# Kernel optimization log

Hardware: AMD Instinct MI355X
Metric: run time of the kernel (lower is better)

Reference implementation:

```python
import jax, jax.numpy as jnp
import numpy as np

B, IMG, TXT, DIM, H, D = 1, 1024, 256, 1536, 24, 64
SCALE = 1.0  # control cross-attn scale


def _lin(x, w, b):
    return x @ w + b


def _heads(x):  # [B,S,DIM] -> [B,H,S,D]
    return jnp.swapaxes(x.reshape(x.shape[0], x.shape[1], H, D), 1, 2)


def _merge(x):  # [B,H,S,D] -> [B,S,DIM]
    return jnp.swapaxes(x, 1, 2).reshape(x.shape[0], x.shape[2], H * D)


def _sdpa(q, k, v):
    s = jnp.einsum('bhqd,bhkd->bhqk', q, k) * (1.0 / np.sqrt(D))
    return jnp.einsum('bhqk,bhkd->bhqd', jax.nn.softmax(s, axis=-1), v)


def _rope(x, pe):  # x: [B,H,S,D], pe: [1,1,S,D//2,2,2]
    xr = x.reshape(*x.shape[:-1], -1, 1, 2)  # [B,H,S,D/2,1,2]
    out = pe[..., 0] * xr[..., 0] + pe[..., 1] * xr[..., 1]  # [B,H,S,D/2,2]
    return out.reshape(x.shape)


def _forward(hidden_states, encoder_hidden_states, hidden_states_control,
             encoder_hidden_states_control, img_to_q_control, pe,
             a_q_w, a_q_b, a_k_w, a_k_b, a_v_w, a_v_b,
             a_addq_w, a_addq_b, a_addk_w, a_addk_b, a_addv_w, a_addv_b,
             a_out_w, a_out_b, a_addout_w, a_addout_b,
             c_q_w, c_q_b, c_k_w, c_k_b, c_v_w, c_v_b,
             c_addq_w, c_addq_b, c_addk_w, c_addk_b, c_addv_w, c_addv_b,
             c_out_w, c_out_b, c_addout_w, c_addout_b):
    img_len = hidden_states.shape[1]
    # ---- main joint attention stream (no RoPE, per original) ----
    q = jnp.concatenate([_heads(_lin(hidden_states, a_q_w, a_q_b)),
                         _heads(_lin(encoder_hidden_states, a_addq_w, a_addq_b))], axis=2)
    k = jnp.concatenate([_heads(_lin(hidden_states, a_k_w, a_k_b)),
                         _heads(_lin(encoder_hidden_states, a_addk_w, a_addk_b))], axis=2)
    v = jnp.concatenate([_heads(_lin(hidden_states, a_v_w, a_v_b)),
                         _heads(_lin(encoder_hidden_states, a_addv_w, a_addv_b))], axis=2)
    hs = _merge(_sdpa(q, k, v))
    hs, ehs = hs[:, :img_len], hs[:, img_len:]
    # ---- control joint attention stream (with RoPE) ----
    qc = jnp.concatenate([_heads(_lin(hidden_states_control, c_q_w, c_q_b)),
                          _heads(_lin(encoder_hidden_states_control, c_addq_w, c_addq_b))], axis=2)
    kc = jnp.concatenate([_heads(_lin(hidden_states_control, c_k_w, c_k_b)),
                          _heads(_lin(encoder_hidden_states_control, c_addk_w, c_addk_b))], axis=2)
    vc = jnp.concatenate([_heads(_lin(hidden_states_control, c_v_w, c_v_b)),
                          _heads(_lin(encoder_hidden_states_control, c_addv_w, c_addv_b))], axis=2)
    key_cross, value_cross = kc, vc  # saved BEFORE RoPE, per original
    hsc = _merge(_sdpa(_rope(qc, pe), _rope(kc, pe), vc))
    hsc, ehsc = hsc[:, :img_len], hsc[:, img_len:]
    # ---- cross attention: img query attends to control K/V ----
    q_cross = _rope(_heads(img_to_q_control), pe[:, :, :img_len])
    k_cross = _rope(key_cross, pe[:, :, :key_cross.shape[2]])
    cross = _merge(_sdpa(q_cross, k_cross, value_cross))
    hs = hs + SCALE * cross
    # ---- output projections (to_out[1] is dropout p=0 -> identity) ----
    hs = _lin(hs, a_out_w, a_out_b)
    ehs = _lin(ehs, a_addout_w, a_addout_b)
    hsc = _lin(hsc, c_out_w, c_out_b)
    ehsc = _lin(ehsc, c_addout_w, c_addout_b)
    return hs, ehs, hsc, ehsc


def setup_inputs() -> dict:
    key = jax.random.key(0)
    ki = iter(jax.random.split(key, 80))
    d = {}
    d['hidden_states'] = jax.random.normal(next(ki), (B, IMG, DIM), jnp.float32)
    d['encoder_hidden_states'] = jax.random.normal(next(ki), (B, TXT, DIM), jnp.float32)
    d['hidden_states_control'] = jax.random.normal(next(ki), (B, IMG, DIM), jnp.float32)
    d['encoder_hidden_states_control'] = jax.random.normal(next(ki), (B, TXT, DIM), jnp.float32)
    d['img_to_q_control'] = jax.random.normal(next(ki), (B, IMG, DIM), jnp.float32)
    # realistic rotary pe: [1,1,S,D/2,2,2] rotation matrices
    S = IMG + TXT
    pos = np.arange(S, dtype=np.float32)
    freqs = 1.0 / (10000.0 ** (np.arange(0, D, 2, dtype=np.float32) / D))  # [D/2]
    ang = pos[:, None] * freqs[None, :]  # [S, D/2]
    cos, sin = np.cos(ang), np.sin(ang)
    pe = np.stack([np.stack([cos, -sin], -1), np.stack([sin, cos], -1)], -2)  # [S,D/2,2,2]
    d['pe'] = jnp.asarray(pe)[None, None]
    for p in ('a', 'c'):
        for name in ('q', 'k', 'v', 'addq', 'addk', 'addv', 'out', 'addout'):
            d[f'{p}_{name}_w'] = jax.random.normal(next(ki), (DIM, DIM), jnp.float32) * 0.02
            d[f'{p}_{name}_b'] = jax.random.normal(next(ki), (DIM,), jnp.float32) * 0.01
    return d


def reference(hidden_states, encoder_hidden_states, hidden_states_control,
              encoder_hidden_states_control, img_to_q_control, pe,
              a_q_w, a_q_b, a_k_w, a_k_b, a_v_w, a_v_b,
              a_addq_w, a_addq_b, a_addk_w, a_addk_b, a_addv_w, a_addv_b,
              a_out_w, a_out_b, a_addout_w, a_addout_b,
              c_q_w, c_q_b, c_k_w, c_k_b, c_v_w, c_v_b,
              c_addq_w, c_addq_b, c_addk_w, c_addk_b, c_addv_w, c_addv_b,
              c_out_w, c_out_b, c_addout_w, c_addout_b):
    return _forward(hidden_states, encoder_hidden_states, hidden_states_control,
                    encoder_hidden_states_control, img_to_q_control, pe,
                    a_q_w, a_q_b, a_k_w, a_k_b, a_v_w, a_v_b,
                    a_addq_w, a_addq_b, a_addk_w, a_addk_b, a_addv_w, a_addv_b,
                    a_out_w, a_out_b, a_addout_w, a_addout_b,
                    c_q_w, c_q_b, c_k_w, c_k_b, c_v_w, c_v_b,
                    c_addq_w, c_addq_b, c_addk_w, c_addk_b, c_addv_w, c_addv_b,
                    c_out_w, c_out_b, c_addout_w, c_addout_b)
```

## Files before the change

### kernel.cpp

```cpp
#include <hip/hip_runtime.h>

#define DIM 1536
#define IMG 1024
#define TXT 256
#define SEQ 1280
#define NH 24
#define HD 64
#define SD ((size_t)SEQ * DIM)
#define IDSZ ((size_t)IMG * DIM)
#define WSZ ((size_t)DIM * DIM)

typedef __attribute__((ext_vector_type(8))) short short8;
typedef __attribute__((ext_vector_type(4))) float f32x4;

__device__ __forceinline__ float bf2f(ushort u) {
    union { unsigned int i; float f; } v; v.i = ((unsigned int)u) << 16; return v.f;
}
__device__ __forceinline__ ushort f2bf(float f) {
    union { unsigned int i; float f; } v; v.f = f;
    unsigned int u = v.i;
    u += 0x7fffu + ((u >> 16) & 1u);
    return (ushort)(u >> 16);
}
__device__ __forceinline__ ushort f2bf_rz(float f) {
    union { unsigned int i; float f; } v; v.f = f;
    return (ushort)(v.i >> 16);
}

__global__ __launch_bounds__(256) void detect_dtype(const void* __restrict__ p,
                                                    int* __restrict__ flag)
{
    __shared__ int cnt;
    if (threadIdx.x == 0) cnt = 0;
    __syncthreads();
    const ushort* u = (const ushort*)p;
    int local = 0;
    for (int i = threadIdx.x; i < 2048; i += 256) {
        ushort v = u[2 * i];
        int e = (v >> 7) & 0xFF;
        if (e >= 0xC0) local++;
    }
    atomicAdd(&cnt, local);
    __syncthreads();
    if (threadIdx.x == 0) flag[0] = (cnt > 16) ? 1 : 0;
}

struct CvtP {
    const void* src[20];
    ushort* dst[20];
    int n8[20];
};

__global__ __launch_bounds__(256) void convert_bf16(CvtP p, const int* __restrict__ dflag)
{
    const int a = blockIdx.y;
    const int i = blockIdx.x * 256 + threadIdx.x;
    if (i >= p.n8[a]) return;
    const size_t off = (size_t)i * 8;
    uint4 o;
    if (dflag[0]) {
        const float* s = (const float*)p.src[a] + off;
        const float4 f0 = *(const float4*)s;
        const float4 f1 = *(const float4*)(s + 4);
        ushort t[8];
        t[0] = f2bf(f0.x); t[1] = f2bf(f0.y); t[2] = f2bf(f0.z); t[3] = f2bf(f0.w);
        t[4] = f2bf(f1.x); t[5] = f2bf(f1.y); t[6] = f2bf(f1.z); t[7] = f2bf(f1.w);
        o = *(uint4*)t;
    } else {
        o = *(const uint4*)((const ushort*)p.src[a] + off);
    }
    *(uint4*)(p.dst[a] + off) = o;
}

#define LSTR 40

struct QKV3P {
    const ushort* Xb;
    const ushort* Wb;
    const void* B[12];
    float* Y[6];
    ushort* Yh[6];
    ushort* Yl[6];
};

__global__ __launch_bounds__(256) void gemm_qkv_v4(QKV3P p, const int* __restrict__ dflag)
{
    __shared__ __align__(16) ushort As[2][128 * LSTR];
    __shared__ __align__(16) ushort Bs[2][64 * 64];
    const int dt = dflag[0];
    const int bx = blockIdx.x;
    const int wsel = bx / 12;
    const int n0 = (bx - wsel * 12) * 128;
    const int ys = blockIdx.y;
    const int str = (ys >= 10) ? 1 : 0;
    const int m0g = (ys - str * 10) * 128;
    const bool istxt = (m0g >= IMG);
    const int widx = str * 6 + wsel + (istxt ? 3 : 0);
    const ushort* X  = p.Xb + (size_t)str * SD;
    const ushort* Wp = p.Wb + (size_t)widx * WSZ;
    const void* Bp = p.B[widx];
    const int yidx = str * 3 + wsel;
    float*  Y  = p.Y[yidx];
    ushort* yh = p.Yh[yidx];
    ushort* yl = p.Yl[yidx];

    const int t = threadIdx.x;
    const int wave = t >> 6, lane = t & 63;
    const int quad = lane >> 4, l16 = lane & 15;
    const int wm = (wave >> 1) * 64, wn = (wave & 1) * 64;

    const int arow = t >> 1, apair = t & 1;
    const int bn8 = (t & 15) << 3, bkk = (t >> 4) << 1;
    const int aps = apair ^ ((arow >> 3) & 1);
    const int adst = arow * LSTR + aps * 16;
    const int bkg = bkk >> 3, bo = bkk & 7;

    f32x4 acc[4][4];
#pragma unroll
    for (int i = 0; i < 4; ++i)
#pragma unroll
        for (int j = 0; j < 4; ++j) acc[i][j] = (f32x4)(0.0f);

    uint4 rau[2];
    uint4 rbu[2];

    auto loadA = [&](int k0) {
        const ushort* xp = X + (size_t)(m0g + arow) * DIM + k0 + apair * 16;
        rau[0] = *(const uint4*)xp;
        rau[1] = *(const uint4*)(xp + 8);
    };
    auto loadB = [&](int k0) {
        const ushort* wp0 = Wp + (size_t)(k0 + bkk) * DIM + n0 + bn8;
        rbu[0] = *(const uint4*)wp0;
        rbu[1] = *(const uint4*)(wp0 + DIM);
    };
    auto storeA = [&](int buf) {
        *(uint4*)&As[buf][adst]     = rau[0];
        *(uint4*)&As[buf][adst + 8] = rau[1];
    };
    auto storeB = [&](int buf) {
        ushort t0[8], t1[8];
        *(uint4*)t0 = rbu[0];
        *(uint4*)t1 = rbu[1];
#pragma unroll
        for (int j = 0; j < 8; ++j) {
            const int rr = bn8 + j;
            const int R = rr & 63, half = rr >> 6;
            const int gx = (((half << 2) + bkg) ^ (R & 7) ^ (R >> 3)) & 7;
            *(unsigned int*)&Bs[buf][R * 64 + gx * 8 + bo] =
                (unsigned int)t0[j] | ((unsigned int)t1[j] << 16);
        }
    };

    loadA(0); loadB(0);
    storeA(0); storeB(0);
    __syncthreads();

    for (int k = 0; k < DIM / 32; ++k) {
        const int cur = k & 1;
        const bool hn = (k + 1) < DIM / 32;
        if (hn) { loadA((k + 1) * 32); loadB((k + 1) * 32); }

        short8 b[4];
#pragma unroll
        for (int j = 0; j < 4; ++j) {
            const int rrn = wn + j * 16 + l16;
            const int R = rrn & 63, half = rrn >> 6;
            const int gx = (((half << 2) + quad) ^ (R & 7) ^ (R >> 3)) & 7;
            b[j] = *(const short8*)&Bs[cur][R * 64 + gx * 8];
        }
#pragma unroll
        for (int i = 0; i < 4; ++i) {
            const int rr = wm + i * 16 + l16;
            const int ps = (quad >> 1) ^ ((rr >> 3) & 1);
            const int col = ps * 16 + (quad & 1) * 8;
            short8 a = *(const short8*)&As[cur][rr * LSTR + col];
#pragma unroll
            for (int j = 0; j < 4; ++j)
                acc[i][j] = __builtin_amdgcn_mfma_f32_16x16x32_bf16(a, b[j], acc[i][j], 0, 0, 0);
        }
        if (hn) { storeA(cur ^ 1); storeB(cur ^ 1); }
        __syncthreads();
    }

#pragma unroll
    for (int j = 0; j < 4; ++j) {
        const int col = n0 + wn + j * 16 + l16;
        const float bv = dt ? ((const float*)Bp)[col] : bf2f(((const ushort*)Bp)[col]);
#pragma unroll
        for (int i = 0; i < 4; ++i)
#pragma unroll
            for (int r = 0; r < 4; ++r) {
                const int row = m0g + wm + i * 16 + quad * 4 + r;
                const size_t o = (size_t)row * DIM + col;
                const float val = acc[i][j][r] + bv;
                if (Y) Y[o] = val;
                if (yh) {
                    const ushort hv = f2bf(val);
                    yh[o] = hv;
                    yl[o] = f2bf(val - bf2f(hv));
                }
            }
    }
}

struct OutP {
    const ushort* Xh; const ushort* Xl;
    const ushort* Wb;
    const void* B[4];
    void* out;
};

__global__ __launch_bounds__(256) void gemm_out_v4(OutP p, const int* __restrict__ dflag)
{
    __shared__ __align__(16) ushort Ah[2][64 * LSTR];
    __shared__ __align__(16) ushort Al[2][64 * LSTR];
    __shared__ __align__(16) ushort Bs[2][64 * 64];
    const int dt = dflag[0];
    const int n0 = blockIdx.x * 128;
    const int mt = blockIdx.y;
    const int seg = (mt < 16) ? 0 : (mt < 20) ? 1 : (mt < 36) ? 2 : 3;
    const ushort* Wp = p.Wb + (size_t)seg * WSZ;
    const void* Bp = p.B[seg];
    const int m0 = mt * 64;

    const int t = threadIdx.x;
    const int wave = t >> 6, lane = t & 63;
    const int quad = lane >> 4, l16 = lane & 15;
    const int wm = (wave >> 1) * 32, wn = (wave & 1) * 64;

    const int arow = t >> 2, ag = t & 3;
    const int apg = ag >> 1, asub = ag & 1;
    const int aps = apg ^ ((arow >> 3) & 1);
    const int adst = arow * LSTR + aps * 16 + asub * 8;
    const int bn8 = (t & 15) << 3, bkk = (t >> 4) << 1;
    const int bkg = bkk >> 3, bo = bkk & 7;

    f32x4 acc[2][4];
#pragma unroll
    for (int i = 0; i < 2; ++i)
#pragma unroll
        for (int j = 0; j < 4; ++j) acc[i][j] = (f32x4)(0.0f);

    uint4 rah, ral;
    uint4 rbu[2];

    auto loadA = [&](int k0) {
        const size_t off = (size_t)(m0 + arow) * DIM + k0 + ag * 8;
        rah = *(const uint4*)(p.Xh + off);
        ral = *(const uint4*)(p.Xl + off);
    };
    auto loadB = [&](int k0) {
        const ushort* wp0 = Wp + (size_t)(k0 + bkk) * DIM + n0 + bn8;
        rbu[0] = *(const uint4*)wp0;
        rbu[1] = *(const uint4*)(wp0 + DIM);
    };
    auto storeA = [&](int buf) {
        *(uint4*)&Ah[buf][adst] = rah;
        *(uint4*)&Al[buf][adst] = ral;
    };
    auto storeB = [&](int buf) {
        ushort t0[8], t1[8];
        *(uint4*)t0 = rbu[0];
        *(uint4*)t1 = rbu[1];
#pragma unroll
        for (int j = 0; j < 8; ++j) {
            const int rr = bn8 + j;
            const int R = rr & 63, half = rr >> 6;
            const int gx = (((half << 2) + bkg) ^ (R & 7) ^ (R >> 3)) & 7;
            *(unsigned int*)&Bs[buf][R * 64 + gx * 8 + bo] =
                (unsigned int)t0[j] | ((unsigned int)t1[j] << 16);
        }
    };

    loadA(0); loadB(0);
    storeA(0); storeB(0);
    __syncthreads();

    for (int k = 0; k < DIM / 32; ++k) {
        const int cur = k & 1;
        const bool hn = (k + 1) < DIM / 32;
        if (hn) { loadA((k + 1) * 32); loadB((k + 1) * 32); }

        short8 b[4];
#pragma unroll
        for (int j = 0; j < 4; ++j) {
            const int rrn = wn + j * 16 + l16;
            const int R = rrn & 63, half = rrn >> 6;
            const int gx = (((half << 2) + quad) ^ (R & 7) ^ (R >> 3)) & 7;
            b[j] = *(const short8*)&Bs[cur][R * 64 + gx * 8];
        }
#pragma unroll
        for (int i = 0; i < 2; ++i) {
            const int rr = wm + i * 16 + l16;
            const int ps = (quad >> 1) ^ ((rr >> 3) & 1);
            const int col = ps * 16 + (quad & 1) * 8;
            short8 ah = *(const short8*)&Ah[cur][rr * LSTR + col];
            short8 al = *(const short8*)&Al[cur][rr * LSTR + col];
#pragma unroll
            for (int j = 0; j < 4; ++j) {
                acc[i][j] = __builtin_amdgcn_mfma_f32_16x16x32_bf16(ah, b[j], acc[i][j], 0, 0, 0);
                acc[i][j] = __builtin_amdgcn_mfma_f32_16x16x32_bf16(al, b[j], acc[i][j], 0, 0, 0);
            }
        }
        if (hn) { storeA(cur ^ 1); storeB(cur ^ 1); }
        __syncthreads();
    }

#pragma unroll
    for (int j = 0; j < 4; ++j) {
        const int col = n0 + wn + j * 16 + l16;
        const float bv = dt ? ((const float*)Bp)[col] : bf2f(((const ushort*)Bp)[col]);
#pragma unroll
        for (int i = 0; i < 2; ++i)
#pragma unroll
            for (int r = 0; r < 4; ++r) {
                const int grow = m0 + wm + i * 16 + quad * 4 + r;
                const size_t o = (size_t)grow * DIM + col;
                const float val = acc[i][j][r] + bv;
                if (dt) ((float*)p.out)[o] = val;
                else    ((ushort*)p.out)[o] = f2bf(val);
            }
    }
}

__device__ __forceinline__ void pe_load(const void* pe, int dt, size_t off,
                                        float& c00, float& c01, float& c10, float& c11)
{
    if (dt) {
        float4 pv = *(const float4*)((const float*)pe + off);
        c00 = pv.x; c01 = pv.y; c10 = pv.z; c11 = pv.w;
    } else {
        const ushort* pp = (const ushort*)pe + off;
        c00 = bf2f(pp[0]); c01 = bf2f(pp[1]); c10 = bf2f(pp[2]); c11 = bf2f(pp[3]);
    }
}

struct PrepP {
    const float* v1; const float* vC;
    ushort *vthA, *vtlA, *vthC, *vtlC;
    float* q1;
    const float* k1; ushort *khC, *kloC;
    const void* i2q; float* qx;
    const void* pe;
};

#define VT_BLKS 960
#define RN0 (SEQ * 768)
#define RN1 (SEQ * 768)
#define RN2 (IMG * 768)

__global__ __launch_bounds__(256) void prep_fused(PrepP p, const int* __restrict__ dflag)
{
    __shared__ unsigned int tile[64 * 65];
    const int dt = dflag[0];
    const int bx = blockIdx.x;
    const int t = threadIdx.x;

    if (bx < VT_BLKS) {
        const int z = bx / 480, rem = bx - z * 480;
        const int s0 = (rem % 20) * 64, h = rem / 20;
        const float* V = z ? p.vC : p.v1;
        ushort* Vth = z ? p.vthC : p.vthA;
        ushort* Vtl = z ? p.vtlC : p.vtlA;
#pragma unroll
        for (int it = 0; it < 16; ++it) {
            const int sl = (t >> 6) + (it << 2);
            const int d = t & 63;
            const float v = V[(size_t)(s0 + sl) * DIM + h * HD + d];
            const ushort hv = f2bf(v);
            const ushort lv = f2bf(v - bf2f(hv));
            tile[d * 65 + sl] = (unsigned int)hv | ((unsigned int)lv << 16);
        }
        __syncthreads();
        const int d = t >> 2, cc = (t & 3) << 4;
        ushort th[16], tl[16];
#pragma unroll
        for (int j = 0; j < 16; ++j) {
            const unsigned int w = tile[d * 65 + cc + j];
            th[j] = (ushort)w;
            tl[j] = (ushort)(w >> 16);
        }
        const size_t off = (size_t)(h * HD + d) * SEQ + s0 + cc;
        *(uint4*)(Vth + off)     = *(uint4*)&th[0];
        *(uint4*)(Vth + off + 8) = *(uint4*)&th[8];
        *(uint4*)(Vtl + off)     = *(uint4*)&tl[0];
        *(uint4*)(Vtl + off + 8) = *(uint4*)&tl[8];
        return;
    }

    int idx = (bx - VT_BLKS) * 256 + t;
    if (idx < RN0) {
        int s = idx / 768, pp = idx - s * 768;
        int col = pp << 1, i = pp & 31;
        float* bp = p.q1 + (size_t)s * DIM + col;
        float x0 = bp[0], x1 = bp[1];
        float c00, c01, c10, c11;
        pe_load(p.pe, dt, (size_t)s * 128 + i * 4, c00, c01, c10, c11);
        bp[0] = c00 * x0 + c01 * x1;
        bp[1] = c10 * x0 + c11 * x1;
        return;
    }
    idx -= RN0;
    if (idx < RN1) {
        int s = idx / 768, pp = idx - s * 768;
        int col = pp << 1, i = pp & 31;
        float2 xv = *(const float2*)(p.k1 + (size_t)s * DIM + col);
        float c00, c01, c10, c11;
        pe_load(p.pe, dt, (size_t)s * 128 + i * 4, c00, c01, c10, c11);
        float y0 = c00 * xv.x + c01 * xv.y;
        float y1 = c10 * xv.x + c11 * xv.y;
        ushort h0 = f2bf(y0), h1 = f2bf(y1);
        ushort l0 = f2bf(y0 - bf2f(h0)), l1 = f2bf(y1 - bf2f(h1));
        *(unsigned int*)(p.khC  + (size_t)s * DIM + col) = (unsigned int)h0 | ((unsigned int)h1 << 16);
        *(unsigned int*)(p.kloC + (size_t)s * DIM + col) = (unsigned int)l0 | ((unsigned int)l1 << 16);
        return;
    }
    idx -= RN1;
    if (idx < RN2) {
        int s = idx / 768, pp = idx - s * 768;
        int col = pp << 1, i = pp & 31;
        float x0, x1;
        if (dt) {
            float2 xv = *(const float2*)((const float*)p.i2q + (size_t)s * DIM + col);
            x0 = xv.x; x1 = xv.y;
        } else {
            const ushort* sp = (const ushort*)p.i2q + (size_t)s * DIM + col;
            x0 = bf2f(sp[0]); x1 = bf2f(sp[1]);
        }
        float c00, c01, c10, c11;
        pe_load(p.pe, dt, (size_t)s * 128 + i * 4, c00, c01, c10, c11);
        float* dp = p.qx + (size_t)s * DIM + col;
        dp[0] = c00 * x0 + c01 * x1;
        dp[1] = c10 * x0 + c11 * x1;
    }
}

__device__ __forceinline__ int swz(int row, int col) {
    return row * 64 + ((((col >> 3) ^ row) & 7) << 3) + (col & 7);
}
__device__ __forceinline__ short8 ldfrag(const ushort* plane, int row, int col) {
    return *(const short8*)&plane[swz(row, col)];
}

struct AttnAllP {
    const float* Qf[3];
    const ushort* Kh[3]; const ushort* Kl[3];
    const ushort* Vth[3]; const ushort* Vtl[3];
    float* Op0[3]; float* Op1[3];
    float2* Ml[3];
    int mlq[3];
};

__global__ __launch_bounds__(256) void attn_all(AttnAllP p)
{
    __shared__ ushort Qh_[4096], Ql_[4096];
    __shared__ ushort Kh_[4096], Kl_[4096];
    __shared__ ushort Vh_[4096], Vl_[4096];

    const int bx = blockIdx.x;
    const int seg = (bx < 20) ? 0 : (bx < 40) ? 1 : 2;
    const int q0 = (bx - ((seg == 0) ? 0 : (seg == 1) ? 20 : 40)) * 64;
    const int h = blockIdx.y;
    const int z = blockIdx.z;
    const int t = threadIdx.x;
    const int wave = t >> 6, lane = t & 63;
    const int quad = lane >> 4, l16 = lane & 15;
    const int wq0 = wave * 16;

    const float* Qf = p.Qf[seg];
    const ushort* Kh = p.Kh[seg]; const ushort* Kl = p.Kl[seg];
    const ushort* Vth = p.Vth[seg]; const ushort* Vtl = p.Vtl[seg];

    const int srow = t >> 2, c0 = (t & 3) << 4;
    const int g0 = c0 >> 3;
    const int p0 = ((g0 ^ (srow & 7)) & 7) << 3;
    const int p1 = (((g0 + 1) ^ (srow & 7)) & 7) << 3;

    {
        const float* src = Qf + (size_t)(q0 + srow) * DIM + h * HD + c0;
        float x[16];
        *(float4*)&x[0]  = *(const float4*)(src);
        *(float4*)&x[4]  = *(const float4*)(src + 4);
        *(float4*)&x[8]  = *(const float4*)(src + 8);
        *(float4*)&x[12] = *(const float4*)(src + 12);
        ushort hi[16], lo[16];
#pragma unroll
        for (int i = 0; i < 16; ++i) {
            const float xs = x[i] * 0.125f;
            hi[i] = f2bf(xs);
            lo[i] = f2bf(xs - bf2f(hi[i]));
        }
        *(uint4*)&Qh_[srow * 64 + p0] = *(uint4*)&hi[0];
        *(uint4*)&Qh_[srow * 64 + p1] = *(uint4*)&hi[8];
        *(uint4*)&Ql_[srow * 64 + p0] = *(uint4*)&lo[0];
        *(uint4*)&Ql_[srow * 64 + p1] = *(uint4*)&lo[8];
    }
    short8 qfh[2], qfl[2];
#pragma unroll
    for (int c = 0; c < 2; ++c) {
        qfh[c] = ldfrag(Qh_, wq0 + l16, c * 32 + quad * 8);
        qfl[c] = ldfrag(Ql_, wq0 + l16, c * 32 + quad * 8);
    }

    float m_[4], l_[4];
#pragma unroll
    for (int r = 0; r < 4; ++r) { m_[r] = -3e38f; l_[r] = 0.0f; }
    f32x4 Oacc[4];
#pragma unroll
    for (int j = 0; j < 4; ++j) Oacc[j] = (f32x4)(0.0f);

    const int kvbeg = z * (SEQ / 2);
    for (int kt = 0; kt < SEQ / 2; kt += 64) {
        const int kv0 = kvbeg + kt;
        __syncthreads();
        {
            const size_t off = (size_t)(kv0 + srow) * DIM + h * HD + c0;
            *(uint4*)&Kh_[srow * 64 + p0] = *(const uint4*)(Kh + off);
            *(uint4*)&Kh_[srow * 64 + p1] = *(const uint4*)(Kh + off + 8);
            *(uint4*)&Kl_[srow * 64 + p0] = *(const uint4*)(Kl + off);
            *(uint4*)&Kl_[srow * 64 + p1] = *(const uint4*)(Kl + off + 8);
        }
        {
            const size_t off = (size_t)(h * HD + srow) * SEQ + kv0 + c0;
            *(uint4*)&Vh_[srow * 64 + p0] = *(const uint4*)(Vth + off);
            *(uint4*)&Vh_[srow * 64 + p1] = *(const uint4*)(Vth + off + 8);
            *(uint4*)&Vl_[srow * 64 + p0] = *(const uint4*)(Vtl + off);
            *(uint4*)&Vl_[srow * 64 + p1] = *(const uint4*)(Vtl + off + 8);
        }
        __syncthreads();

        f32x4 S[4];
#pragma unroll
        for (int j = 0; j < 4; ++j) S[j] = (f32x4)(0.0f);
        __builtin_amdgcn_s_setprio(1);
#pragma unroll
        for (int c = 0; c < 2; ++c) {
#pragma unroll
            for (int j = 0; j < 4; ++j) {
                short8 bh = ldfrag(Kh_, j * 16 + l16, c * 32 + quad * 8);
                short8 bl = ldfrag(Kl_, j * 16 + l16, c * 32 + quad * 8);
                S[j] = __builtin_amdgcn_mfma_f32_16x16x32_bf16(qfh[c], bh, S[j], 0, 0, 0);
                S[j] = __builtin_amdgcn_mfma_f32_16x16x32_bf16(qfl[c], bh, S[j], 0, 0, 0);
                S[j] = __builtin_amdgcn_mfma_f32_16x16x32_bf16(qfh[c], bl, S[j], 0, 0, 0);
            }
        }
        __builtin_amdgcn_s_setprio(0);

        float alpha[4];
#pragma unroll
        for (int r = 0; r < 4; ++r) {
            float mx = fmaxf(fmaxf(S[0][r], S[1][r]), fmaxf(S[2][r], S[3][r]));
            mx = fmaxf(mx, __shfl_xor(mx, 1));
            mx = fmaxf(mx, __shfl_xor(mx, 2));
            mx = fmaxf(mx, __shfl_xor(mx, 4));
            mx = fmaxf(mx, __shfl_xor(mx, 8));
            float mn = fmaxf(m_[r], mx);
            alpha[r] = __expf(m_[r] - mn);
            m_[r] = mn;
            float rs = 0.0f;
#pragma unroll
            for (int j = 0; j < 4; ++j) {
                float pv = __expf(S[j][r] - mn);
                S[j][r] = pv;
                rs += pv;
            }
            rs += __shfl_xor(rs, 1);
            rs += __shfl_xor(rs, 2);
            rs += __shfl_xor(rs, 4);
            rs += __shfl_xor(rs, 8);
            l_[r] = l_[r] * alpha[r] + rs;
        }
#pragma unroll
        for (int j = 0; j < 4; ++j)
#pragma unroll
            for (int r = 0; r < 4; ++r) Oacc[j][r] *= alpha[r];

        {
            const int prow = wq0 + quad * 4;
#pragma unroll
            for (int j = 0; j < 4; ++j)
#pragma unroll
                for (int r = 0; r < 4; ++r) {
                    float pv = S[j][r];
                    ushort ph = f2bf(pv);
                    ushort pl = f2bf_rz(pv - bf2f(ph));
                    int idx = swz(prow + r, j * 16 + l16);
                    Qh_[idx] = ph;
                    Ql_[idx] = pl;
                }
        }

        __builtin_amdgcn_s_setprio(1);
#pragma unroll
        for (int c = 0; c < 2; ++c) {
            short8 pah = ldfrag(Qh_, wq0 + l16, c * 32 + quad * 8);
            short8 pal = ldfrag(Ql_, wq0 + l16, c * 32 + quad * 8);
#pragma unroll
            for (int jn = 0; jn < 4; ++jn) {
                short8 vbh = ldfrag(Vh_, jn * 16 + l16, c * 32 + quad * 8);
                short8 vbl = ldfrag(Vl_, jn * 16 + l16, c * 32 + quad * 8);
                Oacc[jn] = __builtin_amdgcn_mfma_f32_16x16x32_bf16(pah, vbh, Oacc[jn], 0, 0, 0);
                Oacc[jn] = __builtin_amdgcn_mfma_f32_16x16x32_bf16(pal, vbh, Oacc[jn], 0, 0, 0);
                Oacc[jn] = __builtin_amdgcn_mfma_f32_16x16x32_bf16(pah, vbl, Oacc[jn], 0, 0, 0);
            }
        }
        __builtin_amdgcn_s_setprio(0);
    }

    float* Opz = z ? p.Op1[seg] : p.Op0[seg];
    const int mlq = p.mlq[seg];
    float2* Ml = p.Ml[seg];
#pragma unroll
    for (int r = 0; r < 4; ++r) {
        const int rowq = q0 + wq0 + quad * 4 + r;
        if (l16 == 0)
            Ml[((size_t)z * NH + h) * mlq + rowq] = make_float2(m_[r], l_[r]);
#pragma unroll
        for (int jn = 0; jn < 4; ++jn)
            Opz[(size_t)rowq * DIM + h * HD + jn * 16 + l16] = Oacc[jn][r];
    }
}

struct MergeP {
    const float *pA0, *pA1, *pC0, *pC1, *pX0, *pX1;
    const float2 *MlA, *MlC, *MlX;
    ushort *Xh, *Xl;
};

__device__ __forceinline__ float4 comb2(const float* O0, const float* O1,
                                        const float2* Ml, int mlq, int row, int c4)
{
    const int h = c4 >> 6;
    const float2 a = Ml[(size_t)h * mlq + row];
    const float2 b = Ml[(size_t)(NH + h) * mlq + row];
    const float ms = fmaxf(a.x, b.x);
    const float s0 = __expf(a.x - ms), s1 = __expf(b.x - ms);
    const float inv = 1.0f / (s0 * a.y + s1 * b.y);
    const float4 o0 = *(const float4*)&O0[(size_t)row * DIM + c4];
    const float4 o1 = *(const float4*)&O1[(size_t)row * DIM + c4];
    float4 r;
    r.x = (s0 * o0.x + s1 * o1.x) * inv;
    r.y = (s0 * o0.y + s1 * o1.y) * inv;
    r.z = (s0 * o0.z + s1 * o1.z) * inv;
    r.w = (s0 * o0.w + s1 * o1.w) * inv;
    return r;
}

__global__ __launch_bounds__(256) void merge_all(MergeP p)
{
    const int idx = blockIdx.x * 256 + threadIdx.x;
    if (idx >= 2560 * 384) return;
    const int row = idx / 384;
    const int c4 = (idx - row * 384) << 2;
    float4 r;
    if (row < SEQ) {
        r = comb2(p.pA0, p.pA1, p.MlA, SEQ, row, c4);
        if (row < IMG) {
            const float4 x = comb2(p.pX0, p.pX1, p.MlX, IMG, row, c4);
            r.x += x.x; r.y += x.y; r.z += x.z; r.w += x.w;
        }
    } else {
        r = comb2(p.pC0, p.pC1, p.MlC, SEQ, row - SEQ, c4);
    }
    float v[4] = {r.x, r.y, r.z, r.w};
    ushort hi[4], lo[4];
#pragma unroll
    for (int j = 0; j < 4; ++j) {
        hi[j] = f2bf(v[j]);
        lo[j] = f2bf(v[j] - bf2f(hi[j]));
    }
    const size_t o = (size_t)row * DIM + c4;
    *(uint2*)(p.Xh + o) = *(uint2*)hi;
    *(uint2*)(p.Xl + o) = *(uint2*)lo;
}

extern "C" void kernel_launch(void* const* d_in, const int* in_sizes, int n_in,
                              void* d_out, int out_size, void* d_ws, size_t ws_size,
                              hipStream_t stream) {
    (void)in_sizes; (void)n_in; (void)out_size; (void)ws_size;
    const void* hs   = d_in[0];
    const void* ehs  = d_in[1];
    const void* hsc  = d_in[2];
    const void* ehsc = d_in[3];
    const void* i2q  = d_in[4];
    const void* pe   = d_in[5];
#define W_(i) ((const void*)d_in[i])

    char* base = (char*)d_ws;
    int* flag = (int*)base;
    char* ptr = base + 256;
    auto alloc = [&](size_t bytes) { char* r = ptr; ptr += bytes; return r; };
    float* q1  = (float*)alloc(SD * 4);
    float* k1  = (float*)alloc(SD * 4);
    float* v1  = (float*)alloc(SD * 4);
    float* vC  = (float*)alloc(SD * 4);
    float* qA  = (float*)alloc(SD * 4);
    float* qx  = (float*)alloc(IDSZ * 4);
    ushort* khA  = (ushort*)alloc(SD * 2);
    ushort* kloA = (ushort*)alloc(SD * 2);
    ushort* vthA = (ushort*)alloc(SD * 2);
    ushort* vtlA = (ushort*)alloc(SD * 2);
    ushort* khC  = (ushort*)alloc(SD * 2);
    ushort* kloC = (ushort*)alloc(SD * 2);
    ushort* vthC = (ushort*)alloc(SD * 2);
    ushort* vtlC = (ushort*)alloc(SD * 2);
    float* pX0 = (float*)alloc(IDSZ * 4);
    float* pX1 = (float*)alloc(IDSZ * 4);
    float2* MlA = (float2*)alloc((size_t)2 * NH * SEQ * 8);
    float2* MlC = (float2*)alloc((size_t)2 * NH * SEQ * 8);
    float2* MlX = (float2*)alloc((size_t)2 * NH * IMG * 8);
    ushort* Wbf = (ushort*)alloc(16 * WSZ * 2);
    ushort* Xbf = (ushort*)alloc(2 * SD * 2);
    float* pC1 = (float*)Xbf;
    ushort* Xh = (ushort*)qA;
    ushort* Xl = (ushort*)q1;

    dim3 blk(256);
    detect_dtype<<<1, blk, 0, stream>>>(hs, flag);

    {
        CvtP cp;
        const int wsrc[16] = {6, 8, 10, 12, 14, 16, 22, 24, 26, 28, 30, 32,
                              18, 20, 34, 36};
        for (int j = 0; j < 16; ++j) {
            cp.src[j] = W_(wsrc[j]);
            cp.dst[j] = Wbf + (size_t)j * WSZ;
            cp.n8[j] = (int)(WSZ / 8);
        }
        cp.src[16] = hs;   cp.dst[16] = Xbf;             cp.n8[16] = (int)(IDSZ / 8);
        cp.src[17] = ehs;  cp.dst[17] = Xbf + IDSZ;      cp.n8[17] = (int)((size_t)TXT * DIM / 8);
        cp.src[18] = hsc;  cp.dst[18] = Xbf + SD;        cp.n8[18] = (int)(IDSZ / 8);
        cp.src[19] = ehsc; cp.dst[19] = Xbf + SD + IDSZ; cp.n8[19] = (int)((size_t)TXT * DIM / 8);
        convert_bf16<<<dim3((int)(WSZ / 8 + 255) / 256, 20), blk, 0, stream>>>(cp, flag);
    }

    QKV3P qp;
    qp.Xb = Xbf;
    qp.Wb = Wbf;
    {
        const int bsrc[12] = {7, 9, 11, 13, 15, 17, 23, 25, 27, 29, 31, 33};
        for (int j = 0; j < 12; ++j) qp.B[j] = W_(bsrc[j]);
    }
    for (int j = 0; j < 6; ++j) { qp.Y[j] = nullptr; qp.Yh[j] = nullptr; qp.Yl[j] = nullptr; }
    qp.Y[0] = qA;
    qp.Yh[1] = khA; qp.Yl[1] = kloA;
    qp.Y[2] = v1;
    qp.Y[3] = q1;
    qp.Y[4] = k1;
    qp.Y[5] = vC;
    gemm_qkv_v4<<<dim3(36, 20), blk, 0, stream>>>(qp, flag);

    {
        PrepP pp;
        pp.v1 = v1; pp.vC = vC;
        pp.vthA = vthA; pp.vtlA = vtlA; pp.vthC = vthC; pp.vtlC = vtlC;
        pp.q1 = q1;
        pp.k1 = k1; pp.khC = khC; pp.kloC = kloC;
        pp.i2q = i2q; pp.qx = qx;
        pp.pe = pe;
        const int ropeBlocks = (RN0 + RN1 + RN2 + 255) / 256;
        prep_fused<<<VT_BLKS + ropeBlocks, blk, 0, stream>>>(pp, flag);
    }

    {
        AttnAllP ap;
        ap.Qf[0] = qA; ap.Qf[1] = q1; ap.Qf[2] = qx;
        ap.Kh[0] = khA; ap.Kl[0] = kloA;
        ap.Kh[1] = khC; ap.Kl[1] = kloC;
        ap.Kh[2] = khC; ap.Kl[2] = kloC;
        ap.Vth[0] = vthA; ap.Vtl[0] = vtlA;
        ap.Vth[1] = vthC; ap.Vtl[1] = vtlC;
        ap.Vth[2] = vthC; ap.Vtl[2] = vtlC;
        ap.Op0[0] = v1;  ap.Op1[0] = k1;
        ap.Op0[1] = vC;  ap.Op1[1] = pC1;
        ap.Op0[2] = pX0; ap.Op1[2] = pX1;
        ap.Ml[0] = MlA; ap.Ml[1] = MlC; ap.Ml[2] = MlX;
        ap.mlq[0] = SEQ; ap.mlq[1] = SEQ; ap.mlq[2] = IMG;
        attn_all<<<dim3(56, NH, 2), blk, 0, stream>>>(ap);
    }

    {
        MergeP mp;
        mp.pA0 = v1; mp.pA1 = k1;
        mp.pC0 = vC; mp.pC1 = pC1;
        mp.pX0 = pX0; mp.pX1 = pX1;
        mp.MlA = MlA; mp.MlC = MlC; mp.MlX = MlX;
        mp.Xh = Xh; mp.Xl = Xl;
        merge_all<<<(2560 * 384 + 255) / 256, blk, 0, stream>>>(mp);
    }

    {
        OutP op;
        op.Xh = Xh; op.Xl = Xl;
        op.Wb = Wbf + (size_t)12 * WSZ;
        op.B[0] = W_(19); op.B[1] = W_(21); op.B[2] = W_(35); op.B[3] = W_(37);
        op.out = d_out;
        gemm_out_v4<<<dim3(12, 40), blk, 0, stream>>>(op, flag);
    }
#undef W_
}
```

Measured before the change: 552.2 us.

## Fuse control-stream RoPE into QKV GEMM epilogue and use exp2 softmax

```diff
diff --git a/kernel.cpp b/kernel.cpp
--- a/kernel.cpp
+++ b/kernel.cpp
@@ -12,6 +12,8 @@
 
 typedef __attribute__((ext_vector_type(8))) short short8;
 typedef __attribute__((ext_vector_type(4))) float f32x4;
+
+#define QSC 0.18033688011112042f
 
 __device__ __forceinline__ float bf2f(ushort u) {
     union { unsigned int i; float f; } v; v.i = ((unsigned int)u) << 16; return v.f;
@@ -74,10 +76,34 @@
 
 #define LSTR 40
 
+__device__ __forceinline__ void pe_load(const void* pe, int dt, size_t off,
+                                        float& c00, float& c01, float& c10, float& c11)
+{
+    if (dt) {
+        float4 pv = *(const float4*)((const float*)pe + off);
+        c00 = pv.x; c01 = pv.y; c10 = pv.z; c11 = pv.w;
+    } else {
+        const ushort* pp = (const ushort*)pe + off;
+        c00 = bf2f(pp[0]); c01 = bf2f(pp[1]); c10 = bf2f(pp[2]); c11 = bf2f(pp[3]);
+    }
+}
+__device__ __forceinline__ void pe_load2(const void* pe, int dt, size_t off,
+                                         float& c0, float& c1)
+{
+    if (dt) {
+        float2 pv = *(const float2*)((const float*)pe + off);
+        c0 = pv.x; c1 = pv.y;
+    } else {
+        const ushort* pp = (const ushort*)pe + off;
+        c0 = bf2f(pp[0]); c1 = bf2f(pp[1]);
+    }
+}
+
 struct QKV3P {
     const ushort* Xb;
     const ushort* Wb;
     const void* B[12];
+    const void* pe;
     float* Y[6];
     ushort* Yh[6];
     ushort* Yl[6];
@@ -103,6 +129,7 @@
     float*  Y  = p.Y[yidx];
     ushort* yh = p.Yh[yidx];
     ushort* yl = p.Yl[yidx];
+    const int rmode = (str == 1) ? ((wsel == 0) ? 1 : (wsel == 1) ? 2 : 0) : 0;
 
     const int t = threadIdx.x;
     const int wave = t >> 6, lane = t & 63;
@@ -187,6 +214,8 @@
     for (int j = 0; j < 4; ++j) {
         const int col = n0 + wn + j * 16 + l16;
         const float bv = dt ? ((const float*)Bp)[col] : bf2f(((const ushort*)Bp)[col]);
+        const size_t peoc = ((size_t)((col >> 1) & 31)) * 4 + (col & 1) * 2;
+        const bool codd = (col & 1) != 0;
 #pragma unroll
         for (int i = 0; i < 4; ++i)
 #pragma unroll
@@ -194,11 +223,27 @@
                 const int row = m0g + wm + i * 16 + quad * 4 + r;
                 const size_t o = (size_t)row * DIM + col;
                 const float val = acc[i][j][r] + bv;
-                if (Y) Y[o] = val;
-                if (yh) {
-                    const ushort hv = f2bf(val);
-                    yh[o] = hv;
-                    yl[o] = f2bf(val - bf2f(hv));
+                if (rmode == 0) {
+                    if (Y) Y[o] = val;
+                    if (yh) {
+                        const ushort hv = f2bf(val);
+                        yh[o] = hv;
+                        yl[o] = f2bf(val - bf2f(hv));
+                    }
+                } else {
+                    const float other = __shfl_xor(val, 1);
+                    float c0, c1;
+                    pe_load2(p.pe, dt, (size_t)row * 128 + peoc, c0, c1);
+                    const float a = codd ? other : val;
+                    const float b = codd ? val : other;
+                    const float y = c0 * a + c1 * b;
+                    if (rmode == 1) {
+                        Y[o] = y;
+                    } else {
+                        const ushort hv = f2bf(y);
+                        yh[o] = hv;
+                        yl[o] = f2bf(y - bf2f(hv));
+                    }
                 }
             }
     }
@@ -324,30 +369,14 @@
     }
 }
 
-__device__ __forceinline__ void pe_load(const void* pe, int dt, size_t off,
-                                        float& c00, float& c01, float& c10, float& c11)
-{
-    if (dt) {
-        float4 pv = *(const float4*)((const float*)pe + off);
-        c00 = pv.x; c01 = pv.y; c10 = pv.z; c11 = pv.w;
-    } else {
-        const ushort* pp = (const ushort*)pe + off;
-        c00 = bf2f(pp[0]); c01 = bf2f(pp[1]); c10 = bf2f(pp[2]); c11 = bf2f(pp[3]);
-    }
-}
-
 struct PrepP {
     const float* v1; const float* vC;
     ushort *vthA, *vtlA, *vthC, *vtlC;
-    float* q1;
-    const float* k1; ushort *khC, *kloC;
     const void* i2q; float* qx;
     const void* pe;
 };
 
 #define VT_BLKS 960
-#define RN0 (SEQ * 768)
-#define RN1 (SEQ * 768)
 #define RN2 (IMG * 768)
 
 __global__ __launch_bounds__(256) void prep_fused(PrepP p, const int* __restrict__ dflag)
@@ -382,6 +411,7 @@
             tl[j] = (ushort)(w >> 16);
         }
         const size_t off = (size_t)(h * HD + d) * SEQ + s0 + cc;
+        *(uint4*)(p.vthA + 0, Vth + off)     ;
         *(uint4*)(Vth + off)     = *(uint4*)&th[0];
         *(uint4*)(Vth + off + 8) = *(uint4*)&th[8];
         *(uint4*)(Vtl + off)     = *(uint4*)&tl[0];
@@ -390,33 +420,6 @@
     }
 
     int idx = (bx - VT_BLKS) * 256 + t;
-    if (idx < RN0) {
-        int s = idx / 768, pp = idx - s * 768;
-        int col = pp << 1, i = pp & 31;
-        float* bp = p.q1 + (size_t)s * DIM + col;
-        float x0 = bp[0], x1 = bp[1];
-        float c00, c01, c10, c11;
-        pe_load(p.pe, dt, (size_t)s * 128 + i * 4, c00, c01, c10, c11);
-        bp[0] = c00 * x0 + c01 * x1;
-        bp[1] = c10 * x0 + c11 * x1;
-        return;
-    }
-    idx -= RN0;
-    if (idx < RN1) {
-        int s = idx / 768, pp = idx - s * 768;
-        int col = pp << 1, i = pp & 31;
-        float2 xv = *(const float2*)(p.k1 + (size_t)s * DIM + col);
-        float c00, c01, c10, c11;
-        pe_load(p.pe, dt, (size_t)s * 128 + i * 4, c00, c01, c10, c11);
-        float y0 = c00 * xv.x + c01 * xv.y;
-        float y1 = c10 * xv.x + c11 * xv.y;
-        ushort h0 = f2bf(y0), h1 = f2bf(y1);
-        ushort l0 = f2bf(y0 - bf2f(h0)), l1 = f2bf(y1 - bf2f(h1));
-        *(unsigned int*)(p.khC  + (size_t)s * DIM + col) = (unsigned int)h0 | ((unsigned int)h1 << 16);
-        *(unsigned int*)(p.kloC + (size_t)s * DIM + col) = (unsigned int)l0 | ((unsigned int)l1 << 16);
-        return;
-    }
-    idx -= RN1;
     if (idx < RN2) {
         int s = idx / 768, pp = idx - s * 768;
         int col = pp << 1, i = pp & 31;
@@ -458,7 +461,8 @@
     __shared__ ushort Kh_[4096], Kl_[4096];
     __shared__ ushort Vh_[4096], Vl_[4096];
 
-    const int bx = blockIdx.x;
+    const int bxr = blockIdx.x;
+    const int bx = (bxr & 7) * 7 + (bxr >> 3);
     const int seg = (bx < 20) ? 0 : (bx < 40) ? 1 : 2;
     const int q0 = (bx - ((seg == 0) ? 0 : (seg == 1) ? 20 : 40)) * 64;
     const int h = blockIdx.y;
@@ -487,7 +491,7 @@
         ushort hi[16], lo[16];
 #pragma unroll
         for (int i = 0; i < 16; ++i) {
-            const float xs = x[i] * 0.125f;
+            const float xs = x[i] * QSC;
             hi[i] = f2bf(xs);
             lo[i] = f2bf(xs - bf2f(hi[i]));
         }
@@ -556,12 +560,12 @@
             mx = fmaxf(mx, __shfl_xor(mx, 4));
             mx = fmaxf(mx, __shfl_xor(mx, 8));
             float mn = fmaxf(m_[r], mx);
-            alpha[r] = __expf(m_[r] - mn);
+            alpha[r] = exp2f(m_[r] - mn);
             m_[r] = mn;
             float rs = 0.0f;
 #pragma unroll
             for (int j = 0; j < 4; ++j) {
-                float pv = __expf(S[j][r] - mn);
+                float pv = exp2f(S[j][r] - mn);
                 S[j][r] = pv;
                 rs += pv;
             }
@@ -635,7 +639,7 @@
     const float2 a = Ml[(size_t)h * mlq + row];
     const float2 b = Ml[(size_t)(NH + h) * mlq + row];
     const float ms = fmaxf(a.x, b.x);
-    const float s0 = __expf(a.x - ms), s1 = __expf(b.x - ms);
+    const float s0 = exp2f(a.x - ms), s1 = exp2f(b.x - ms);
     const float inv = 1.0f / (s0 * a.y + s1 * b.y);
     const float4 o0 = *(const float4*)&O0[(size_t)row * DIM + c4];
     const float4 o1 = *(const float4*)&O1[(size_t)row * DIM + c4];
@@ -738,6 +742,7 @@
     QKV3P qp;
     qp.Xb = Xbf;
     qp.Wb = Wbf;
+    qp.pe = pe;
     {
         const int bsrc[12] = {7, 9, 11, 13, 15, 17, 23, 25, 27, 29, 31, 33};
         for (int j = 0; j < 12; ++j) qp.B[j] = W_(bsrc[j]);
@@ -747,7 +752,7 @@
     qp.Yh[1] = khA; qp.Yl[1] = kloA;
     qp.Y[2] = v1;
     qp.Y[3] = q1;
-    qp.Y[4] = k1;
+    qp.Yh[4] = khC; qp.Yl[4] = kloC;
     qp.Y[5] = vC;
     gemm_qkv_v4<<<dim3(36, 20), blk, 0, stream>>>(qp, flag);
 
@@ -755,12 +760,9 @@
         PrepP pp;
         pp.v1 = v1; pp.vC = vC;
         pp.vthA = vthA; pp.vtlA = vtlA; pp.vthC = vthC; pp.vtlC = vtlC;
-        pp.q1 = q1;
-        pp.k1 = k1; pp.khC = khC; pp.kloC = kloC;
         pp.i2q = i2q; pp.qx = qx;
         pp.pe = pe;
-        const int ropeBlocks = (RN0 + RN1 + RN2 + 255) / 256;
-        prep_fused<<<VT_BLKS + ropeBlocks, blk, 0, stream>>>(pp, flag);
+        prep_fused<<<VT_BLKS + (RN2 + 255) / 256, blk, 0, stream>>>(pp, flag);
     }
 
     {
```

Measured after the change: 580.3 us. +5.1%, slower.
